# Optimization experiments

Measured on AMD Instinct MI355X. Metric: run time of the kernel, lower is better.

## Reference

```python
import jax, jax.numpy as jnp
import numpy as np
import math

MODEL_DIM = 1024
B, S = 4, 2048


def setup_inputs() -> dict:
    key = jax.random.key(0)
    k_x, k_q, k_k, k_v = jax.random.split(key, 4)
    r5 = math.sqrt(5)
    x = jax.random.normal(k_x, (B, S, MODEL_DIM), dtype=jnp.float32)
    Q = jax.random.uniform(k_q, (MODEL_DIM, MODEL_DIM), minval=-r5, maxval=r5, dtype=jnp.float32)
    K = jax.random.uniform(k_k, (MODEL_DIM, MODEL_DIM), minval=-r5, maxval=r5, dtype=jnp.float32)
    V = jax.random.uniform(k_v, (MODEL_DIM, MODEL_DIM), minval=-r5, maxval=r5, dtype=jnp.float32)
    # attention_input == 'both' -> a == model_dim -> F is the full identity
    F = jnp.eye(MODEL_DIM, dtype=jnp.float32)
    return {"x": x, "Q": Q, "K": K, "V": V, "F": F}


def reference(x, Q, K, V, F):
    d = x.shape[-1]
    xf = jnp.matmul(x, F)
    Qx = jnp.matmul(xf, Q)          # [B,S,D]
    Kx = jnp.matmul(xf, K)          # [B,S,D]
    Vx = jnp.matmul(x, V)           # [B,S,D]
    scores = jnp.einsum('bqd,bkd->bqk', Qx, Kx) / math.sqrt(d)  # [B,S,S]
    seq = x.shape[1]
    mask = jnp.triu(jnp.ones((seq, seq), dtype=bool), k=1)
    scores = jnp.where(mask, -jnp.inf, scores)
    probs = jax.nn.softmax(scores, axis=-1)
    out = jnp.matmul(probs, Vx)     # [B,S,D]
    return (out, probs)
```

## Files before the change

### kernel.cpp

```cpp
#include <hip/hip_runtime.h>
#include <hip/hip_fp16.h>

typedef _Float16 f16;
typedef __attribute__((ext_vector_type(8))) _Float16 f16x8;
typedef __attribute__((ext_vector_type(4))) _Float16 f16x4;
typedef __attribute__((ext_vector_type(4))) float    f32x4;

#define D_MODEL 1024
#define SEQ     2048
#define BATCH   4
#define M_TOT   (BATCH * SEQ)
#define NE      ((long)M_TOT * D_MODEL)
#define WE      ((long)D_MODEL * D_MODEL)
#define OUT_ELEMS  ((long)M_TOT * D_MODEL)

static __device__ __forceinline__ f16x8 frag_read(const f16* lds, int row, int c)
{
    const f16x8* L = (const f16x8*)lds;
    return L[row * 4 + (c ^ ((row >> 1) & 3))];
}

static __device__ __forceinline__ void stage_tile(const f16* __restrict__ g, int row0,
                                                  int ld, int k0, f16* ldsbase,
                                                  int wave, int lane)
{
#pragma unroll
    for (int j = 0; j < 2; ++j) {
        const int chunk = wave * 2 + j;
        const int off16 = chunk * 64 + lane;
        const int row   = off16 >> 2;
        const int slot  = (off16 & 3) ^ ((row >> 1) & 3);
        const f16* src = g + (long)(row0 + row) * ld + (k0 + slot * 8);
        f16* dst = ldsbase + chunk * 512;
        __builtin_amdgcn_global_load_lds((const __attribute__((address_space(1))) void*)src,
                                         (__attribute__((address_space(3))) void*)dst,
                                         16, 0, 0);
    }
}

template<int ROWS>
static __device__ __forceinline__ void stage8(const f16* __restrict__ g, int row0,
                                              int ld, int k0, f16* dstbase,
                                              int wave, int lane)
{
#pragma unroll
    for (int j = 0; j < ROWS / 128; ++j) {
        const int off16 = j * 512 + wave * 64 + lane;
        const int row   = off16 >> 2;
        const int slot  = (off16 & 3) ^ ((row >> 1) & 3);
        const f16* src = g + (long)(row0 + row) * ld + (k0 + slot * 8);
        f16* dst = dstbase + (j * 512 + wave * 64) * 8;
        __builtin_amdgcn_global_load_lds((const __attribute__((address_space(1))) void*)src,
                                         (__attribute__((address_space(3))) void*)dst,
                                         16, 0, 0);
    }
}

#define BUFE 24576

template<int DUAL>
static __device__ __forceinline__ void g8_issueA(const f16* Ah, const f16* Al, int ld,
                                                 int m0, f16* lds, int t, int wave, int lane)
{
    f16* b = lds + (t & 1) * BUFE;
    stage8<256>(Ah, m0, ld, t * 32, b, wave, lane);
    if constexpr (DUAL) stage8<256>(Al, m0, ld, t * 32, b + 8192, wave, lane);
}
static __device__ __forceinline__ void g8_issueBh(const f16* BTh, int ld, int n0,
                                                  f16* lds, int t, int wave, int lane)
{
    stage8<128>(BTh, n0, ld, t * 32, lds + (t & 1) * BUFE + 16384, wave, lane);
}
static __device__ __forceinline__ void g8_issueBl(const f16* BTl, int ld, int n0,
                                                  f16* lds, int t, int wave, int lane)
{
    stage8<128>(BTl, n0, ld, t * 32, lds + (t & 1) * BUFE + 20480, wave, lane);
}

template<int DUAL>
static __device__ __forceinline__ void gemm8_pipe(
    const f16* __restrict__ Ah, const f16* __restrict__ Al,
    const f16* __restrict__ BTh, const f16* __restrict__ BTl,
    int ld, int m0, int n0, int nT, f16* lds, f32x4 acc[4][4], int wave, int lane)
{
    const int wr = wave >> 1, wc = wave & 1;
    const int cf = lane >> 4;

#pragma unroll
    for (int mi = 0; mi < 4; ++mi)
#pragma unroll
        for (int ni = 0; ni < 4; ++ni) acc[mi][ni] = (f32x4){0.f, 0.f, 0.f, 0.f};

    g8_issueA<DUAL>(Ah, Al, ld, m0, lds, 0, wave, lane);
    g8_issueBh(BTh, ld, n0, lds, 0, wave, lane);
    if constexpr (DUAL) g8_issueBl(BTl, ld, n0, lds, 0, wave, lane);
    g8_issueA<DUAL>(Ah, Al, ld, m0, lds, 1, wave, lane);
    g8_issueBh(BTh, ld, n0, lds, 1, wave, lane);

    for (int t = 0; t < nT; ++t) {
        if (t < nT - 1) {
            if constexpr (DUAL) {
                g8_issueBl(BTl, ld, n0, lds, t + 1, wave, lane);
                asm volatile("s_waitcnt vmcnt(6)" ::: "memory");
            } else {
                asm volatile("s_waitcnt vmcnt(3)" ::: "memory");
            }
        } else {
            asm volatile("s_waitcnt vmcnt(0)" ::: "memory");
        }
        __builtin_amdgcn_sched_barrier(0);
        __builtin_amdgcn_s_barrier();
        __builtin_amdgcn_sched_barrier(0);

        f16* buf = lds + (t & 1) * BUFE;
        f16x8 fah[4], fal[4], fbh[4], fbl[4];
#pragma unroll
        for (int i = 0; i < 4; ++i) {
            const int ra = wr * 64 + i * 16 + (lane & 15);
            fah[i] = frag_read(buf, ra, cf);
            if constexpr (DUAL) fal[i] = frag_read(buf + 8192, ra, cf);
            const int rb = wc * 64 + i * 16 + (lane & 15);
            fbh[i] = frag_read(buf + 16384, rb, cf);
            if constexpr (DUAL) fbl[i] = frag_read(buf + 20480, rb, cf);
        }
        asm volatile("s_waitcnt lgkmcnt(0)" ::: "memory");
        __builtin_amdgcn_sched_barrier(0);
        __builtin_amdgcn_s_barrier();
        __builtin_amdgcn_sched_barrier(0);

        if (t < nT - 2) {
            g8_issueA<DUAL>(Ah, Al, ld, m0, lds, t + 2, wave, lane);
            g8_issueBh(BTh, ld, n0, lds, t + 2, wave, lane);
        }
        __builtin_amdgcn_sched_barrier(0);

        __builtin_amdgcn_s_setprio(1);
#pragma unroll
        for (int mi = 0; mi < 4; ++mi)
#pragma unroll
            for (int ni = 0; ni < 4; ++ni)
                acc[mi][ni] = __builtin_amdgcn_mfma_f32_16x16x32_f16(fah[mi], fbh[ni], acc[mi][ni], 0, 0, 0);
        if constexpr (DUAL) {
#pragma unroll
            for (int mi = 0; mi < 4; ++mi)
#pragma unroll
                for (int ni = 0; ni < 4; ++ni)
                    acc[mi][ni] = __builtin_amdgcn_mfma_f32_16x16x32_f16(fah[mi], fbl[ni], acc[mi][ni], 0, 0, 0);
#pragma unroll
            for (int mi = 0; mi < 4; ++mi)
#pragma unroll
                for (int ni = 0; ni < 4; ++ni)
                    acc[mi][ni] = __builtin_amdgcn_mfma_f32_16x16x32_f16(fal[mi], fbh[ni], acc[mi][ni], 0, 0, 0);
        }
        __builtin_amdgcn_s_setprio(0);
    }
}

#define BUFE2 32768

static __device__ __forceinline__ void g256_main(const f16* Ah, const f16* Al,
                                                 const f16* BTh, int ld, int m0, int n0,
                                                 f16* lds, int t, int wave, int lane)
{
    f16* b = lds + (t & 1) * BUFE2;
    stage8<256>(Ah,  m0, ld, t * 32, b,         wave, lane);
    stage8<256>(Al,  m0, ld, t * 32, b + 8192,  wave, lane);
    stage8<256>(BTh, n0, ld, t * 32, b + 16384, wave, lane);
}
static __device__ __forceinline__ void g256_bl(const f16* BTl, int ld, int n0,
                                               f16* lds, int t, int wave, int lane)
{
    stage8<256>(BTl, n0, ld, t * 32, lds + (t & 1) * BUFE2 + 24576, wave, lane);
}

static __device__ __forceinline__ void gemm256d(
    const f16* __restrict__ Ah, const f16* __restrict__ Al,
    const f16* __restrict__ BTh, const f16* __restrict__ BTl,
    int ld, int m0, int n0, f16* lds, f32x4 acc[8][4], int wave, int lane)
{
    const int wr = wave >> 2, wc = wave & 3;
    const int cf = lane >> 4;

#pragma unroll
    for (int mi = 0; mi < 8; ++mi)
#pragma unroll
        for (int ni = 0; ni < 4; ++ni) acc[mi][ni] = (f32x4){0.f, 0.f, 0.f, 0.f};

    g256_main(Ah, Al, BTh, ld, m0, n0, lds, 0, wave, lane);
    g256_bl(BTl, ld, n0, lds, 0, wave, lane);
    g256_main(Ah, Al, BTh, ld, m0, n0, lds, 1, wave, lane);

    for (int t = 0; t < 32; ++t) {
        if (t < 31) {
            g256_bl(BTl, ld, n0, lds, t + 1, wave, lane);
            asm volatile("s_waitcnt vmcnt(8)" ::: "memory");
        } else {
            asm volatile("s_waitcnt vmcnt(0)" ::: "memory");
        }
        __builtin_amdgcn_sched_barrier(0);
        __builtin_amdgcn_s_barrier();
        __builtin_amdgcn_sched_barrier(0);

        f16* buf = lds + (t & 1) * BUFE2;
        f16x8 fah[8], fal[8], fbh[4], fbl[4];
#pragma unroll
        for (int mi = 0; mi < 8; ++mi) {
            const int ra = wr * 128 + mi * 16 + (lane & 15);
            fah[mi] = frag_read(buf,        ra, cf);
            fal[mi] = frag_read(buf + 8192, ra, cf);
        }
#pragma unroll
        for (int ni = 0; ni < 4; ++ni) {
            const int rb = wc * 64 + ni * 16 + (lane & 15);
            fbh[ni] = frag_read(buf + 16384, rb, cf);
            fbl[ni] = frag_read(buf + 24576, rb, cf);
        }
        asm volatile("s_waitcnt lgkmcnt(0)" ::: "memory");
        __builtin_amdgcn_sched_barrier(0);
        __builtin_amdgcn_s_barrier();
        __builtin_amdgcn_sched_barrier(0);

        if (t < 30)
            g256_main(Ah, Al, BTh, ld, m0, n0, lds, t + 2, wave, lane);
        __builtin_amdgcn_sched_barrier(0);

        __builtin_amdgcn_s_setprio(1);
#pragma unroll
        for (int mi = 0; mi < 8; ++mi)
#pragma unroll
            for (int ni = 0; ni < 4; ++ni)
                acc[mi][ni] = __builtin_amdgcn_mfma_f32_16x16x32_f16(fah[mi], fbh[ni], acc[mi][ni], 0, 0, 0);
#pragma unroll
        for (int mi = 0; mi < 8; ++mi)
#pragma unroll
            for (int ni = 0; ni < 4; ++ni)
                acc[mi][ni] = __builtin_amdgcn_mfma_f32_16x16x32_f16(fah[mi], fbl[ni], acc[mi][ni], 0, 0, 0);
#pragma unroll
        for (int mi = 0; mi < 8; ++mi)
#pragma unroll
            for (int ni = 0; ni < 4; ++ni)
                acc[mi][ni] = __builtin_amdgcn_mfma_f32_16x16x32_f16(fal[mi], fbh[ni], acc[mi][ni], 0, 0, 0);
        __builtin_amdgcn_s_setprio(0);
    }
}

__global__ __launch_bounds__(512, 2) void k_gemm_T(
    const f16* __restrict__ xh, const f16* __restrict__ xl,
    const f16* __restrict__ WhT, const f16* __restrict__ WlT,
    f16* __restrict__ Th, f16* __restrict__ Tl)
{
    __shared__ __align__(16) f16 lds[49152];
    const int lane = threadIdx.x & 63, wave = threadIdx.x >> 6;
    const int L = blockIdx.x;
    const int swz = (L & 7) * 32 + (L >> 3);
    const int m0 = (swz >> 3) * 256;
    const int n0 = (swz & 7) * 128;
    f32x4 acc[4][4];
    gemm8_pipe<1>(xh, xl, WhT, WlT, D_MODEL, m0, n0, 32, lds, acc, wave, lane);
    const int wr = wave >> 1, wc = wave & 1;
#pragma unroll
    for (int mi = 0; mi < 4; ++mi)
#pragma unroll
        for (int ni = 0; ni < 4; ++ni) {
            const int gn = n0 + wc * 64 + ni * 16 + (lane & 15);
#pragma unroll
            for (int r = 0; r < 4; ++r) {
                const int gm = m0 + wr * 64 + mi * 16 + (lane >> 4) * 4 + r;
                const float v = acc[mi][ni][r];
                const f16 h = (f16)v;
                Th[(long)gm * D_MODEL + gn] = h;
                Tl[(long)gm * D_MODEL + gn] = (f16)(v - (float)h);
            }
        }
}

__global__ __launch_bounds__(512, 2) void k_mega1(
    const f16* __restrict__ Th, const f16* __restrict__ Tl,
    const f16* __restrict__ xh, const f16* __restrict__ xl,
    const f16* __restrict__ VhT,
    float* __restrict__ scores, f16* __restrict__ VxT)
{
    __shared__ __align__(16) f16 lds[65536];
    const int lane = threadIdx.x & 63, wave = threadIdx.x >> 6;

    if (blockIdx.x < 144) {
        const int L = blockIdx.x;
        const int b = L / 36;
        const int t = L - b * 36;
        int qt = (int)((sqrtf(8.f * (float)t + 1.f) - 1.f) * 0.5f);
        while ((qt + 1) * (qt + 2) / 2 <= t) ++qt;
        while (qt * (qt + 1) / 2 > t) --qt;
        const int kt = t - qt * (qt + 1) / 2;

        const long ob = (long)b * SEQ * D_MODEL;
        f32x4 acc[8][4];
        gemm256d(Th + ob, Tl + ob, xh + ob, xl + ob, D_MODEL,
                 qt * 256, kt * 256, lds, acc, wave, lane);

        float* sb = scores + (long)b * SEQ * SEQ;
        const int wr = wave >> 2, wc = wave & 3;
#pragma unroll
        for (int mi = 0; mi < 8; ++mi)
#pragma unroll
            for (int ni = 0; ni < 4; ++ni) {
                const int k = kt * 256 + wc * 64 + ni * 16 + (lane & 15);
#pragma unroll
                for (int r = 0; r < 4; ++r) {
                    const int q = qt * 256 + wr * 128 + mi * 16 + (lane >> 4) * 4 + r;
                    sb[(long)q * SEQ + k] = acc[mi][ni][r] * 0.03125f;
                }
            }
    } else {
        const int idx = blockIdx.x - 144;
        const int m0 = (idx >> 3) * 256;
        const int n0 = (idx & 7) * 128;
        f32x4 acc[4][4];
        gemm8_pipe<0>(xh, nullptr, VhT, nullptr, D_MODEL, m0, n0, 32, lds, acc, wave, lane);
        const int wr = wave >> 1, wc = wave & 1;
#pragma unroll
        for (int mi = 0; mi < 4; ++mi) {
            const int gm0 = m0 + wr * 64 + mi * 16 + (lane >> 4) * 4;
            const int b = gm0 >> 11, s = gm0 & 2047;
#pragma unroll
            for (int ni = 0; ni < 4; ++ni) {
                const int gn = n0 + wc * 64 + ni * 16 + (lane & 15);
                f16x4 p = {(f16)acc[mi][ni][0], (f16)acc[mi][ni][1],
                           (f16)acc[mi][ni][2], (f16)acc[mi][ni][3]};
                *(f16x4*)(VxT + ((long)b * D_MODEL + gn) * SEQ + s) = p;
            }
        }
    }
}

__global__ __launch_bounds__(512, 2) void k_gemm_pv8(
    const f16* __restrict__ P, const f16* __restrict__ VT, float* __restrict__ out)
{
    __shared__ __align__(16) f16 lds[49152];
    const int lane = threadIdx.x & 63, wave = threadIdx.x >> 6;
    const int i = blockIdx.x;
    const int qt = 7 - (i >> 5);
    const int dt = (i >> 2) & 7;
    const int b  = i & 3;
    const int nT = 8 * (qt + 1);
    f32x4 acc[4][4];
    const f16* Pb  = P  + (long)b * SEQ * SEQ;
    const f16* VTb = VT + (long)b * D_MODEL * SEQ;
    gemm8_pipe<0>(Pb, nullptr, VTb, nullptr, SEQ, qt * 256, dt * 128, nT, lds, acc, wave, lane);
    float* ob = out + (long)b * SEQ * D_MODEL;
    const int wr = wave >> 1, wc = wave & 1;
#pragma unroll
    for (int mi = 0; mi < 4; ++mi)
#pragma unroll
        for (int ni = 0; ni < 4; ++ni) {
            const int d = dt * 128 + wc * 64 + ni * 16 + (lane & 15);
#pragma unroll
            for (int r = 0; r < 4; ++r) {
                const int qq = qt * 256 + wr * 64 + mi * 16 + (lane >> 4) * 4 + r;
                ob[(long)qq * D_MODEL + d] = acc[mi][ni][r];
            }
        }
}

static __device__ __forceinline__ void gemm_core_dual(
    const f16* __restrict__ Ah, const f16* __restrict__ Al,
    const f16* __restrict__ BTh, const f16* __restrict__ BTl,
    int ld, int m0, int n0, int kEnd, f16* lds, f32x4 acc[4][4])
{
    const int t = threadIdx.x;
    const int lane = t & 63;
    const int wave = t >> 6;
    const int wr = wave >> 1, wc = wave & 1;
    const int cfrag = lane >> 4;

#pragma unroll
    for (int mi = 0; mi < 4; ++mi)
#pragma unroll
        for (int ni = 0; ni < 4; ++ni)
            acc[mi][ni] = (f32x4){0.f, 0.f, 0.f, 0.f};

    for (int k0 = 0; k0 < kEnd; k0 += 32) {
        stage_tile(Ah,  m0, ld, k0, lds,         wave, lane);
        stage_tile(BTh, n0, ld, k0, lds + 4096,  wave, lane);
        stage_tile(Al,  m0, ld, k0, lds + 8192,  wave, lane);
        stage_tile(BTl, n0, ld, k0, lds + 12288, wave, lane);
        __syncthreads();

        f16x8 fah[4], fbh[4], fal[4], fbl[4];
#pragma unroll
        for (int i = 0; i < 4; ++i) {
            fah[i] = frag_read(lds,         wr * 64 + i * 16 + (lane & 15), cfrag);
            fbh[i] = frag_read(lds + 4096,  wc * 64 + i * 16 + (lane & 15), cfrag);
            fal[i] = frag_read(lds + 8192,  wr * 64 + i * 16 + (lane & 15), cfrag);
            fbl[i] = frag_read(lds + 12288, wc * 64 + i * 16 + (lane & 15), cfrag);
        }
#pragma unroll
        for (int mi = 0; mi < 4; ++mi)
#pragma unroll
            for (int ni = 0; ni < 4; ++ni) {
                acc[mi][ni] = __builtin_amdgcn_mfma_f32_16x16x32_f16(fah[mi], fbh[ni], acc[mi][ni], 0, 0, 0);
                acc[mi][ni] = __builtin_amdgcn_mfma_f32_16x16x32_f16(fah[mi], fbl[ni], acc[mi][ni], 0, 0, 0);
                acc[mi][ni] = __builtin_amdgcn_mfma_f32_16x16x32_f16(fal[mi], fbh[ni], acc[mi][ni], 0, 0, 0);
            }
        __syncthreads();
    }
}

__global__ __launch_bounds__(256) void k_split_all(
    const float* __restrict__ x, const float* __restrict__ Q,
    const float* __restrict__ K, const float* __restrict__ V,
    f16* __restrict__ xh, f16* __restrict__ xl,
    f16* __restrict__ Qh, f16* __restrict__ Ql,
    f16* __restrict__ Kh, f16* __restrict__ Kl,
    f16* __restrict__ VhT)
{
    __shared__ float tile[32][33];
    const int bid = blockIdx.x;
    if (bid < 10240) {
        const float* src; f16 *dh, *dl; long off;
        if (bid < 8192)      { src = x; dh = xh; dl = xl; off = (long)bid * 1024; }
        else if (bid < 9216) { src = Q; dh = Qh; dl = Ql; off = (long)(bid - 8192) * 1024; }
        else                 { src = K; dh = Kh; dl = Kl; off = (long)(bid - 9216) * 1024; }
        const long i = off + threadIdx.x * 4;
        float4 v = *(const float4*)(src + i);
        f16 h0 = (f16)v.x, h1 = (f16)v.y, h2 = (f16)v.z, h3 = (f16)v.w;
        f16x4 hh = {h0, h1, h2, h3};
        f16x4 ll = {(f16)(v.x - (float)h0), (f16)(v.y - (float)h1),
                    (f16)(v.z - (float)h2), (f16)(v.w - (float)h3)};
        *(f16x4*)(dh + i) = hh;
        *(f16x4*)(dl + i) = ll;
    } else {
        const int idx = bid - 10240;
        const int n0 = (idx & 31) * 32, k0 = (idx >> 5) * 32;
        const int c = threadIdx.x & 31, r8 = threadIdx.x >> 5;
#pragma unroll
        for (int i = 0; i < 4; ++i) {
            const int r = r8 + i * 8;
            tile[r][c] = V[(long)(k0 + r) * D_MODEL + n0 + c];
        }
        __syncthreads();
#pragma unroll
        for (int i = 0; i < 4; ++i) {
            const int r = r8 + i * 8;
            VhT[(long)(n0 + r) * D_MODEL + k0 + c] = (f16)tile[c][r];
        }
    }
}

__global__ __launch_bounds__(256, 2) void k_gemm_w(
    const f16* __restrict__ Qh, const f16* __restrict__ Ql,
    const f16* __restrict__ Kh, const f16* __restrict__ Kl,
    f16* __restrict__ WhT, f16* __restrict__ WlT)
{
    __shared__ __align__(16) f16 lds[16384];
    f32x4 acc[4][4];
    const int m0 = blockIdx.y * 128, n0 = blockIdx.x * 128;
    gemm_core_dual(Qh, Ql, Kh, Kl, D_MODEL, m0, n0, D_MODEL, lds, acc);
    const int lane = threadIdx.x & 63, wave = threadIdx.x >> 6;
    const int wr = wave >> 1, wc = wave & 1;
#pragma unroll
    for (int mi = 0; mi < 4; ++mi)
#pragma unroll
        for (int ni = 0; ni < 4; ++ni) {
            const int gn = n0 + wc * 64 + ni * 16 + (lane & 15);
#pragma unroll
            for (int r = 0; r < 4; ++r) {
                const int gm = m0 + wr * 64 + mi * 16 + (lane >> 4) * 4 + r;
                const float v = acc[mi][ni][r];
                const f16 h = (f16)v;
                WhT[(long)gn * D_MODEL + gm] = h;
                WlT[(long)gn * D_MODEL + gm] = (f16)(v - (float)h);
            }
        }
}

__global__ __launch_bounds__(256) void k_softmax(float* __restrict__ probs,
                                                 f16* __restrict__ probs16)
{
    const long row = blockIdx.x;
    const int q = (int)(row & (SEQ - 1));
    float* s = probs + row * SEQ;
    const int t = threadIdx.x;
    const int kb = t * 8;
    float4 u0 = *(const float4*)(s + kb);
    float4 u1 = *(const float4*)(s + kb + 4);
    float v[8] = {u0.x, u0.y, u0.z, u0.w, u1.x, u1.y, u1.z, u1.w};
    float mx = -3.0e38f;
#pragma unroll
    for (int j = 0; j < 8; ++j) if (kb + j <= q) mx = fmaxf(mx, v[j]);
#pragma unroll
    for (int off = 32; off > 0; off >>= 1) mx = fmaxf(mx, __shfl_xor(mx, off, 64));
    __shared__ float redA[4], redB[4];
    const int lane = t & 63, wave = t >> 6;
    if (lane == 0) redA[wave] = mx;
    __syncthreads();
    mx = fmaxf(fmaxf(redA[0], redA[1]), fmaxf(redA[2], redA[3]));
    float e[8]; float sum = 0.f;
#pragma unroll
    for (int j = 0; j < 8; ++j) { e[j] = (kb + j <= q) ? __expf(v[j] - mx) : 0.f; sum += e[j]; }
#pragma unroll
    for (int off = 32; off > 0; off >>= 1) sum += __shfl_xor(sum, off, 64);
    if (lane == 0) redB[wave] = sum;
    __syncthreads();
    sum = (redB[0] + redB[1]) + (redB[2] + redB[3]);
    const float inv = 1.f / sum;
    float4 w0 = {e[0] * inv, e[1] * inv, e[2] * inv, e[3] * inv};
    float4 w1 = {e[4] * inv, e[5] * inv, e[6] * inv, e[7] * inv};
    *(float4*)(s + kb) = w0;
    *(float4*)(s + kb + 4) = w1;
    f16x8 p16 = {(f16)w0.x, (f16)w0.y, (f16)w0.z, (f16)w0.w,
                 (f16)w1.x, (f16)w1.y, (f16)w1.z, (f16)w1.w};
    *(f16x8*)(probs16 + row * SEQ + kb) = p16;
}

extern "C" void kernel_launch(void* const* d_in, const int* in_sizes, int n_in,
                              void* d_out, int out_size, void* d_ws, size_t ws_size,
                              hipStream_t stream)
{
    const float* x = (const float*)d_in[0];
    const float* Q = (const float*)d_in[1];
    const float* K = (const float*)d_in[2];
    const float* V = (const float*)d_in[3];

    float* out   = (float*)d_out;
    float* probs = out + OUT_ELEMS;

    f16* base = (f16*)d_ws;
    f16* xh   = base;
    f16* xl   = base + NE;
    f16* Th   = base + 2 * NE;
    f16* Tl   = base + 3 * NE;
    f16* VxT  = base + 4 * NE;
    f16* Qh   = base + 5 * NE;
    f16* Ql   = Qh + WE;
    f16* Kh   = Qh + 2 * WE;
    f16* Kl   = Qh + 3 * WE;
    f16* WhT  = Qh + 4 * WE;
    f16* WlT  = Qh + 5 * WE;
    f16* VhT  = Qh + 6 * WE;
    f16* probs16 = base + 2 * NE;

    k_split_all<<<11264, 256, 0, stream>>>(x, Q, K, V, xh, xl, Qh, Ql, Kh, Kl, VhT);
    k_gemm_w<<<dim3(8, 8), 256, 0, stream>>>(Qh, Ql, Kh, Kl, WhT, WlT);
    k_gemm_T<<<256, 512, 0, stream>>>(xh, xl, WhT, WlT, Th, Tl);
    k_mega1<<<400, 512, 0, stream>>>(Th, Tl, xh, xl, VhT, probs, VxT);
    k_softmax<<<8192, 256, 0, stream>>>(probs, probs16);
    k_gemm_pv8<<<256, 512, 0, stream>>>(probs16, VxT, out);
}
```

Measured before the change: 259.0 us.

## Interleave LDS fragment reads with MFMAs, shrink PV LDS, nontemporal stores, batch split

Result: no change. 260.1 us (+0.4%).

```diff
diff --git a/kernel.cpp b/kernel.cpp
--- a/kernel.cpp
+++ b/kernel.cpp
@@ -56,25 +56,32 @@
     }
 }
 
-#define BUFE 24576
+template<int DUAL> struct G8 {
+    static constexpr int BUF    = DUAL ? 24576 : 12288;
+    static constexpr int OFF_AL = 8192;
+    static constexpr int OFF_BH = DUAL ? 16384 : 8192;
+    static constexpr int OFF_BL = 20480;
+};
 
 template<int DUAL>
 static __device__ __forceinline__ void g8_issueA(const f16* Ah, const f16* Al, int ld,
                                                  int m0, f16* lds, int t, int wave, int lane)
 {
-    f16* b = lds + (t & 1) * BUFE;
+    f16* b = lds + (t & 1) * G8<DUAL>::BUF;
     stage8<256>(Ah, m0, ld, t * 32, b, wave, lane);
-    if constexpr (DUAL) stage8<256>(Al, m0, ld, t * 32, b + 8192, wave, lane);
-}
+    if constexpr (DUAL) stage8<256>(Al, m0, ld, t * 32, b + G8<DUAL>::OFF_AL, wave, lane);
+}
+template<int DUAL>
 static __device__ __forceinline__ void g8_issueBh(const f16* BTh, int ld, int n0,
                                                   f16* lds, int t, int wave, int lane)
 {
-    stage8<128>(BTh, n0, ld, t * 32, lds + (t & 1) * BUFE + 16384, wave, lane);
-}
+    stage8<128>(BTh, n0, ld, t * 32, lds + (t & 1) * G8<DUAL>::BUF + G8<DUAL>::OFF_BH, wave, lane);
+}
+template<int DUAL>
 static __device__ __forceinline__ void g8_issueBl(const f16* BTl, int ld, int n0,
                                                   f16* lds, int t, int wave, int lane)
 {
-    stage8<128>(BTl, n0, ld, t * 32, lds + (t & 1) * BUFE + 20480, wave, lane);
+    stage8<128>(BTl, n0, ld, t * 32, lds + (t & 1) * G8<DUAL>::BUF + G8<DUAL>::OFF_BL, wave, lane);
 }
 
 template<int DUAL>
@@ -92,15 +99,15 @@
         for (int ni = 0; ni < 4; ++ni) acc[mi][ni] = (f32x4){0.f, 0.f, 0.f, 0.f};
 
     g8_issueA<DUAL>(Ah, Al, ld, m0, lds, 0, wave, lane);
-    g8_issueBh(BTh, ld, n0, lds, 0, wave, lane);
-    if constexpr (DUAL) g8_issueBl(BTl, ld, n0, lds, 0, wave, lane);
+    g8_issueBh<DUAL>(BTh, ld, n0, lds, 0, wave, lane);
+    if constexpr (DUAL) g8_issueBl<DUAL>(BTl, ld, n0, lds, 0, wave, lane);
     g8_issueA<DUAL>(Ah, Al, ld, m0, lds, 1, wave, lane);
-    g8_issueBh(BTh, ld, n0, lds, 1, wave, lane);
+    g8_issueBh<DUAL>(BTh, ld, n0, lds, 1, wave, lane);
 
     for (int t = 0; t < nT; ++t) {
         if (t < nT - 1) {
             if constexpr (DUAL) {
-                g8_issueBl(BTl, ld, n0, lds, t + 1, wave, lane);
+                g8_issueBl<DUAL>(BTl, ld, n0, lds, t + 1, wave, lane);
                 asm volatile("s_waitcnt vmcnt(6)" ::: "memory");
             } else {
                 asm volatile("s_waitcnt vmcnt(3)" ::: "memory");
@@ -112,17 +119,54 @@
         __builtin_amdgcn_s_barrier();
         __builtin_amdgcn_sched_barrier(0);
 
-        f16* buf = lds + (t & 1) * BUFE;
-        f16x8 fah[4], fal[4], fbh[4], fbl[4];
+        f16* buf = lds + (t & 1) * G8<DUAL>::BUF;
+
+        f16x8 fbh[4], fbl[4];
 #pragma unroll
         for (int i = 0; i < 4; ++i) {
-            const int ra = wr * 64 + i * 16 + (lane & 15);
-            fah[i] = frag_read(buf, ra, cf);
-            if constexpr (DUAL) fal[i] = frag_read(buf + 8192, ra, cf);
             const int rb = wc * 64 + i * 16 + (lane & 15);
-            fbh[i] = frag_read(buf + 16384, rb, cf);
-            if constexpr (DUAL) fbl[i] = frag_read(buf + 20480, rb, cf);
-        }
+            fbh[i] = frag_read(buf + G8<DUAL>::OFF_BH, rb, cf);
+            if constexpr (DUAL) fbl[i] = frag_read(buf + G8<DUAL>::OFF_BL, rb, cf);
+        }
+        f16x8 pah[2][2], pal[2][2];
+#pragma unroll
+        for (int j = 0; j < 2; ++j) {
+            const int ra = wr * 64 + j * 16 + (lane & 15);
+            pah[0][j] = frag_read(buf, ra, cf);
+            if constexpr (DUAL) pal[0][j] = frag_read(buf + G8<DUAL>::OFF_AL, ra, cf);
+        }
+#pragma unroll
+        for (int p = 0; p < 2; ++p) {
+            const int cur = p & 1, nxt = cur ^ 1;
+            if (p < 1) {
+#pragma unroll
+                for (int j = 0; j < 2; ++j) {
+                    const int ra = wr * 64 + (2 * (p + 1) + j) * 16 + (lane & 15);
+                    pah[nxt][j] = frag_read(buf, ra, cf);
+                    if constexpr (DUAL) pal[nxt][j] = frag_read(buf + G8<DUAL>::OFF_AL, ra, cf);
+                }
+            }
+            __builtin_amdgcn_s_setprio(1);
+#pragma unroll
+            for (int j = 0; j < 2; ++j)
+#pragma unroll
+                for (int ni = 0; ni < 4; ++ni)
+                    acc[2 * p + j][ni] = __builtin_amdgcn_mfma_f32_16x16x32_f16(pah[cur][j], fbh[ni], acc[2 * p + j][ni], 0, 0, 0);
+            if constexpr (DUAL) {
+#pragma unroll
+                for (int j = 0; j < 2; ++j)
+#pragma unroll
+                    for (int ni = 0; ni < 4; ++ni)
+                        acc[2 * p + j][ni] = __builtin_amdgcn_mfma_f32_16x16x32_f16(pah[cur][j], fbl[ni], acc[2 * p + j][ni], 0, 0, 0);
+#pragma unroll
+                for (int j = 0; j < 2; ++j)
+#pragma unroll
+                    for (int ni = 0; ni < 4; ++ni)
+                        acc[2 * p + j][ni] = __builtin_amdgcn_mfma_f32_16x16x32_f16(pal[cur][j], fbh[ni], acc[2 * p + j][ni], 0, 0, 0);
+            }
+            __builtin_amdgcn_s_setprio(0);
+        }
+
         asm volatile("s_waitcnt lgkmcnt(0)" ::: "memory");
         __builtin_amdgcn_sched_barrier(0);
         __builtin_amdgcn_s_barrier();
@@ -130,29 +174,9 @@
 
         if (t < nT - 2) {
             g8_issueA<DUAL>(Ah, Al, ld, m0, lds, t + 2, wave, lane);
-            g8_issueBh(BTh, ld, n0, lds, t + 2, wave, lane);
-        }
-        __builtin_amdgcn_sched_barrier(0);
-
-        __builtin_amdgcn_s_setprio(1);
-#pragma unroll
-        for (int mi = 0; mi < 4; ++mi)
-#pragma unroll
-            for (int ni = 0; ni < 4; ++ni)
-                acc[mi][ni] = __builtin_amdgcn_mfma_f32_16x16x32_f16(fah[mi], fbh[ni], acc[mi][ni], 0, 0, 0);
-        if constexpr (DUAL) {
-#pragma unroll
-            for (int mi = 0; mi < 4; ++mi)
-#pragma unroll
-                for (int ni = 0; ni < 4; ++ni)
-                    acc[mi][ni] = __builtin_amdgcn_mfma_f32_16x16x32_f16(fah[mi], fbl[ni], acc[mi][ni], 0, 0, 0);
-#pragma unroll
-            for (int mi = 0; mi < 4; ++mi)
-#pragma unroll
-                for (int ni = 0; ni < 4; ++ni)
-                    acc[mi][ni] = __builtin_amdgcn_mfma_f32_16x16x32_f16(fal[mi], fbh[ni], acc[mi][ni], 0, 0, 0);
-        }
-        __builtin_amdgcn_s_setprio(0);
+            g8_issueBh<DUAL>(BTh, ld, n0, lds, t + 2, wave, lane);
+        }
+        __builtin_amdgcn_sched_barrier(0);
     }
 }
 
@@ -202,19 +226,51 @@
         __builtin_amdgcn_sched_barrier(0);
 
         f16* buf = lds + (t & 1) * BUFE2;
-        f16x8 fah[8], fal[8], fbh[4], fbl[4];
-#pragma unroll
-        for (int mi = 0; mi < 8; ++mi) {
-            const int ra = wr * 128 + mi * 16 + (lane & 15);
-            fah[mi] = frag_read(buf,        ra, cf);
-            fal[mi] = frag_read(buf + 8192, ra, cf);
-        }
+
+        f16x8 fbh[4], fbl[4];
 #pragma unroll
         for (int ni = 0; ni < 4; ++ni) {
             const int rb = wc * 64 + ni * 16 + (lane & 15);
             fbh[ni] = frag_read(buf + 16384, rb, cf);
             fbl[ni] = frag_read(buf + 24576, rb, cf);
         }
+        f16x8 pah[2][2], pal[2][2];
+#pragma unroll
+        for (int j = 0; j < 2; ++j) {
+            const int ra = wr * 128 + j * 16 + (lane & 15);
+            pah[0][j] = frag_read(buf,        ra, cf);
+            pal[0][j] = frag_read(buf + 8192, ra, cf);
+        }
+#pragma unroll
+        for (int p = 0; p < 4; ++p) {
+            const int cur = p & 1, nxt = cur ^ 1;
+            if (p < 3) {
+#pragma unroll
+                for (int j = 0; j < 2; ++j) {
+                    const int ra = wr * 128 + (2 * (p + 1) + j) * 16 + (lane & 15);
+                    pah[nxt][j] = frag_read(buf,        ra, cf);
+                    pal[nxt][j] = frag_read(buf + 8192, ra, cf);
+                }
+            }
+            __builtin_amdgcn_s_setprio(1);
+#pragma unroll
+            for (int j = 0; j < 2; ++j)
+#pragma unroll
+                for (int ni = 0; ni < 4; ++ni)
+                    acc[2 * p + j][ni] = __builtin_amdgcn_mfma_f32_16x16x32_f16(pah[cur][j], fbh[ni], acc[2 * p + j][ni], 0, 0, 0);
+#pragma unroll
+            for (int j = 0; j < 2; ++j)
+#pragma unroll
+                for (int ni = 0; ni < 4; ++ni)
+                    acc[2 * p + j][ni] = __builtin_amdgcn_mfma_f32_16x16x32_f16(pah[cur][j], fbl[ni], acc[2 * p + j][ni], 0, 0, 0);
+#pragma unroll
+            for (int j = 0; j < 2; ++j)
+#pragma unroll
+                for (int ni = 0; ni < 4; ++ni)
+                    acc[2 * p + j][ni] = __builtin_amdgcn_mfma_f32_16x16x32_f16(pal[cur][j], fbh[ni], acc[2 * p + j][ni], 0, 0, 0);
+            __builtin_amdgcn_s_setprio(0);
+        }
+
         asm volatile("s_waitcnt lgkmcnt(0)" ::: "memory");
         __builtin_amdgcn_sched_barrier(0);
         __builtin_amdgcn_s_barrier();
@@ -223,24 +279,6 @@
         if (t < 30)
             g256_main(Ah, Al, BTh, ld, m0, n0, lds, t + 2, wave, lane);
         __builtin_amdgcn_sched_barrier(0);
-
-        __builtin_amdgcn_s_setprio(1);
-#pragma unroll
-        for (int mi = 0; mi < 8; ++mi)
-#pragma unroll
-            for (int ni = 0; ni < 4; ++ni)
-                acc[mi][ni] = __builtin_amdgcn_mfma_f32_16x16x32_f16(fah[mi], fbh[ni], acc[mi][ni], 0, 0, 0);
-#pragma unroll
-        for (int mi = 0; mi < 8; ++mi)
-#pragma unroll
-            for (int ni = 0; ni < 4; ++ni)
-                acc[mi][ni] = __builtin_amdgcn_mfma_f32_16x16x32_f16(fah[mi], fbl[ni], acc[mi][ni], 0, 0, 0);
-#pragma unroll
-        for (int mi = 0; mi < 8; ++mi)
-#pragma unroll
-            for (int ni = 0; ni < 4; ++ni)
-                acc[mi][ni] = __builtin_amdgcn_mfma_f32_16x16x32_f16(fal[mi], fbh[ni], acc[mi][ni], 0, 0, 0);
-        __builtin_amdgcn_s_setprio(0);
     }
 }
 
@@ -307,7 +345,8 @@
 #pragma unroll
                 for (int r = 0; r < 4; ++r) {
                     const int q = qt * 256 + wr * 128 + mi * 16 + (lane >> 4) * 4 + r;
-                    sb[(long)q * SEQ + k] = acc[mi][ni][r] * 0.03125f;
+                    __builtin_nontemporal_store(acc[mi][ni][r] * 0.03125f,
+                                                &sb[(long)q * SEQ + k]);
                 }
             }
     } else {
@@ -332,10 +371,10 @@
     }
 }
 
-__global__ __launch_bounds__(512, 2) void k_gemm_pv8(
+__global__ __launch_bounds__(512, 4) void k_gemm_pv8(
     const f16* __restrict__ P, const f16* __restrict__ VT, float* __restrict__ out)
 {
-    __shared__ __align__(16) f16 lds[49152];
+    __shared__ __align__(16) f16 lds[24576];
     const int lane = threadIdx.x & 63, wave = threadIdx.x >> 6;
     const int i = blockIdx.x;
     const int qt = 7 - (i >> 5);
@@ -415,21 +454,24 @@
 {
     __shared__ float tile[32][33];
     const int bid = blockIdx.x;
-    if (bid < 10240) {
-        const float* src; f16 *dh, *dl; long off;
-        if (bid < 8192)      { src = x; dh = xh; dl = xl; off = (long)bid * 1024; }
-        else if (bid < 9216) { src = Q; dh = Qh; dl = Ql; off = (long)(bid - 8192) * 1024; }
-        else                 { src = K; dh = Kh; dl = Kl; off = (long)(bid - 9216) * 1024; }
-        const long i = off + threadIdx.x * 4;
-        float4 v = *(const float4*)(src + i);
-        f16 h0 = (f16)v.x, h1 = (f16)v.y, h2 = (f16)v.z, h3 = (f16)v.w;
-        f16x4 hh = {h0, h1, h2, h3};
-        f16x4 ll = {(f16)(v.x - (float)h0), (f16)(v.y - (float)h1),
-                    (f16)(v.z - (float)h2), (f16)(v.w - (float)h3)};
-        *(f16x4*)(dh + i) = hh;
-        *(f16x4*)(dl + i) = ll;
+    if (bid < 2560) {
+        const float* src; f16 *dh, *dl; long base;
+        if (bid < 2048)      { src = x; dh = xh; dl = xl; base = (long)bid * 4096; }
+        else if (bid < 2304) { src = Q; dh = Qh; dl = Ql; base = (long)(bid - 2048) * 4096; }
+        else                 { src = K; dh = Kh; dl = Kl; base = (long)(bid - 2304) * 4096; }
+#pragma unroll
+        for (int j = 0; j < 4; ++j) {
+            const long i = base + (j * 256 + threadIdx.x) * 4;
+            float4 v = *(const float4*)(src + i);
+            f16 h0 = (f16)v.x, h1 = (f16)v.y, h2 = (f16)v.z, h3 = (f16)v.w;
+            f16x4 hh = {h0, h1, h2, h3};
+            f16x4 ll = {(f16)(v.x - (float)h0), (f16)(v.y - (float)h1),
+                        (f16)(v.z - (float)h2), (f16)(v.w - (float)h3)};
+            *(f16x4*)(dh + i) = hh;
+            *(f16x4*)(dl + i) = ll;
+        }
     } else {
-        const int idx = bid - 10240;
+        const int idx = bid - 2560;
         const int n0 = (idx & 31) * 32, k0 = (idx >> 5) * 32;
         const int c = threadIdx.x & 31, r8 = threadIdx.x >> 5;
 #pragma unroll
@@ -481,9 +523,13 @@
     float* s = probs + row * SEQ;
     const int t = threadIdx.x;
     const int kb = t * 8;
-    float4 u0 = *(const float4*)(s + kb);
-    float4 u1 = *(const float4*)(s + kb + 4);
-    float v[8] = {u0.x, u0.y, u0.z, u0.w, u1.x, u1.y, u1.z, u1.w};
+    float v[8] = {0.f, 0.f, 0.f, 0.f, 0.f, 0.f, 0.f, 0.f};
+    if (kb <= q) {
+        float4 u0 = *(const float4*)(s + kb);
+        float4 u1 = *(const float4*)(s + kb + 4);
+        v[0] = u0.x; v[1] = u0.y; v[2] = u0.z; v[3] = u0.w;
+        v[4] = u1.x; v[5] = u1.y; v[6] = u1.z; v[7] = u1.w;
+    }
     float mx = -3.0e38f;
 #pragma unroll
     for (int j = 0; j < 8; ++j) if (kb + j <= q) mx = fmaxf(mx, v[j]);
@@ -503,10 +549,10 @@
     __syncthreads();
     sum = (redB[0] + redB[1]) + (redB[2] + redB[3]);
     const float inv = 1.f / sum;
-    float4 w0 = {e[0] * inv, e[1] * inv, e[2] * inv, e[3] * inv};
-    float4 w1 = {e[4] * inv, e[5] * inv, e[6] * inv, e[7] * inv};
-    *(float4*)(s + kb) = w0;
-    *(float4*)(s + kb + 4) = w1;
+    f32x4 w0 = {e[0] * inv, e[1] * inv, e[2] * inv, e[3] * inv};
+    f32x4 w1 = {e[4] * inv, e[5] * inv, e[6] * inv, e[7] * inv};
+    __builtin_nontemporal_store(w0, (f32x4*)(s + kb));
+    __builtin_nontemporal_store(w1, (f32x4*)(s + kb + 4));
     f16x8 p16 = {(f16)w0.x, (f16)w0.y, (f16)w0.z, (f16)w0.w,
                  (f16)w1.x, (f16)w1.y, (f16)w1.z, (f16)w1.w};
     *(f16x8*)(probs16 + row * SEQ + kb) = p16;
@@ -539,7 +585,7 @@
     f16* VhT  = Qh + 6 * WE;
     f16* probs16 = base + 2 * NE;
 
-    k_split_all<<<11264, 256, 0, stream>>>(x, Q, K, V, xh, xl, Qh, Ql, Kh, Kl, VhT);
+    k_split_all<<<3584, 256, 0, stream>>>(x, Q, K, V, xh, xl, Qh, Ql, Kh, Kl, VhT);
     k_gemm_w<<<dim3(8, 8), 256, 0, stream>>>(Qh, Ql, Kh, Kl, WhT, WlT);
     k_gemm_T<<<256, 512, 0, stream>>>(xh, xl, WhT, WlT, Th, Tl);
     k_mega1<<<400, 512, 0, stream>>>(Th, Tl, xh, xl, VhT, probs, VxT);
```
